# Kernel tuning notes

Measured on AMD Instinct MI355X. Metric: run time of the kernel, lower is better.

The kernel has to match this reference:

```python
import jax, jax.numpy as jnp
import numpy as np

N_NODES = 100000
N_EDGES = 3200000
D_IN, D_HID, D_OUT = 128, 128, 128


def setup_inputs() -> dict:
    key = jax.random.key(0)
    ks = jax.random.split(key, 8)
    x = jax.random.normal(ks[0], (N_NODES, D_IN), dtype=jnp.float32)
    edge_index = jax.random.randint(ks[1], (2, N_EDGES), 0, N_NODES, dtype=jnp.int64)
    def lin(k, din, dout):
        # glorot-ish init for GCNConv weight
        s = 1.0 / np.sqrt(din)
        return jax.random.uniform(k, (din, dout), jnp.float32, -s, s)
    W0 = lin(ks[2], D_IN, D_HID)
    b0 = jnp.zeros((D_HID,), jnp.float32)
    W1 = lin(ks[3], D_HID, D_HID)
    b1 = jnp.zeros((D_HID,), jnp.float32)
    W2 = lin(ks[4], D_HID, D_OUT)
    b2 = jnp.zeros((D_OUT,), jnp.float32)
    return {"x": x, "edge_index": edge_index, "W0": W0, "b0": b0,
            "W1": W1, "b1": b1, "W2": W2, "b2": b2}


def _gcn_norm(edge_index, n_nodes):
    # PyG gcn_norm with self-loops: deg over target index, sym normalization
    loop = jnp.arange(n_nodes, dtype=edge_index.dtype)
    src = jnp.concatenate([edge_index[0], loop])
    dst = jnp.concatenate([edge_index[1], loop])
    deg = jax.ops.segment_sum(jnp.ones_like(dst, dtype=jnp.float32), dst,
                              num_segments=n_nodes)
    dinv = jnp.where(deg > 0, jax.lax.rsqrt(deg), 0.0)
    norm = dinv[src] * dinv[dst]  # [E + N]
    return src, dst, norm


def _gcn_conv(h, src, dst, norm, W, b, n_nodes):
    h = h @ W                                   # [N, dout] transform first
    msg = h[src] * norm[:, None]                # gather + scale
    out = jax.ops.segment_sum(msg, dst, num_segments=n_nodes)  # scatter-add
    return out + b


def reference(x, edge_index, W0, b0, W1, b1, W2, b2):
    n = x.shape[0]
    src, dst, norm = _gcn_norm(edge_index, n)
    # layer 0
    h = jax.nn.relu(_gcn_conv(x, src, dst, norm, W0, b0, n))
    # residual middle layer (dropout is identity in eval mode)
    h = jax.nn.relu(_gcn_conv(h, src, dst, norm, W1, b1, n) + h)
    # output layer
    return _gcn_conv(h, src, dst, norm, W2, b2, n)
```

## Files before the change

### kernel.cpp

```cpp
#include <hip/hip_runtime.h>
#include <hip/hip_fp16.h>

#define D 128
typedef unsigned long long ull;
typedef _Float16 half8 __attribute__((ext_vector_type(8)));
typedef _Float16 half4v __attribute__((ext_vector_type(4)));
typedef float f32x4 __attribute__((ext_vector_type(4)));

#define KPOS(k4) (((k4) & ~31) + ((((k4) & 15) >> 2) << 3) + ((((k4) >> 4) & 1) << 2))

__global__ void k_zero_int(int* p, int n) {
  int i = blockIdx.x * blockDim.x + threadIdx.x;
  if (i < n) p[i] = 0;
}

__global__ void k_deg_count8(const int* __restrict__ ei, int* __restrict__ deg8,
                             int E, int N) {
  int e = blockIdx.x * blockDim.x + threadIdx.x;
  if (e >= E) return;
  int d = __builtin_nontemporal_load(&ei[E + e]);
  atomicAdd(&deg8[(blockIdx.x & 7) * N + d], 1);
}

__global__ void k_deg_reduce(const int* __restrict__ deg8, int* __restrict__ deg, int N) {
  int i = blockIdx.x * blockDim.x + threadIdx.x;
  if (i >= N) return;
  int s = 0;
#pragma unroll
  for (int c = 0; c < 8; c++) s += deg8[c * N + i];
  deg[i] = s;
}

__global__ void k_scan_part(const int* __restrict__ deg, int* __restrict__ part, int n) {
  __shared__ int sd[256];
  int base = blockIdx.x * 2048 + threadIdx.x * 8;
  int s = 0;
#pragma unroll
  for (int k = 0; k < 8; k++) {
    int idx = base + k;
    if (idx < n) s += deg[idx];
  }
  sd[threadIdx.x] = s;
  __syncthreads();
  for (int off = 128; off > 0; off >>= 1) {
    if (threadIdx.x < off) sd[threadIdx.x] += sd[threadIdx.x + off];
    __syncthreads();
  }
  if (threadIdx.x == 0) part[blockIdx.x] = sd[0];
}

__global__ void k_scan_offsets(int* __restrict__ part, int nparts,
                               int* __restrict__ rowptr, int n) {
  __shared__ int sd[256];
  int v = (threadIdx.x < nparts) ? part[threadIdx.x] : 0;
  sd[threadIdx.x] = v;
  __syncthreads();
  for (int off = 1; off < 256; off <<= 1) {
    int t = (threadIdx.x >= off) ? sd[threadIdx.x - off] : 0;
    __syncthreads();
    sd[threadIdx.x] += t;
    __syncthreads();
  }
  if (threadIdx.x < nparts) part[threadIdx.x] = sd[threadIdx.x] - v;
  if (threadIdx.x == 0) rowptr[n] = sd[255];
}

__global__ void k_scan_final(const int* __restrict__ deg, const int* __restrict__ part,
                             int* __restrict__ rowptr, int n) {
  __shared__ int sd[256];
  int base = blockIdx.x * 2048 + threadIdx.x * 8;
  int loc[8];
  int s = 0;
#pragma unroll
  for (int k = 0; k < 8; k++) {
    int idx = base + k;
    loc[k] = (idx < n) ? deg[idx] : 0;
    s += loc[k];
  }
  sd[threadIdx.x] = s;
  __syncthreads();
  for (int off = 1; off < 256; off <<= 1) {
    int t = (threadIdx.x >= off) ? sd[threadIdx.x - off] : 0;
    __syncthreads();
    sd[threadIdx.x] += t;
    __syncthreads();
  }
  int run = part[blockIdx.x] + sd[threadIdx.x] - s;
#pragma unroll
  for (int k = 0; k < 8; k++) {
    int idx = base + k;
    if (idx < n) {
      rowptr[idx] = run;
      run += loc[k];
    }
  }
}

__global__ void k_dinv_cursor(const int* __restrict__ rowptr, float* __restrict__ dinv,
                              int* __restrict__ cursor, int n) {
  int i = blockIdx.x * blockDim.x + threadIdx.x;
  if (i < n) {
    int r0 = rowptr[i], r1 = rowptr[i + 1];
    dinv[i] = rsqrtf((float)(r1 - r0) + 1.0f);
    cursor[i] = r0;
  }
}

__global__ void k_csr_fill_x(const int* __restrict__ ei, int* __restrict__ cursor,
                             int* __restrict__ csr, int E, int bsz) {
  const int bucket = blockIdx.x & 7;
  const int slice = blockIdx.x >> 3;
  const int nsl = gridDim.x >> 3;
  const int lo = bucket * bsz;
  const int chunk = (E + nsl - 1) / nsl;
  const int start = slice * chunk;
  int endE = start + chunk;
  if (endE > E) endE = E;
  for (int e = start + threadIdx.x; e < endE; e += 256) {
    int d = __builtin_nontemporal_load(&ei[E + e]);
    if ((unsigned)(d - lo) < (unsigned)bsz) {
      int s = __builtin_nontemporal_load(&ei[e]);
      int pos = atomicAdd(&cursor[d], 1);
      csr[pos] = s;
    }
  }
}

template <int HALF_IN>
__launch_bounds__(256, 2)
__global__ void k_gemm_mfma(const void* __restrict__ Av, const float* __restrict__ W,
                            const float* __restrict__ dinv, __half* __restrict__ Th, int n) {
  __shared__ _Float16 Al[128 * 136];
  __shared__ _Float16 Bl[128 * 136];
  const int tid = threadIdx.x;
  const int row0 = blockIdx.x * 128;

  if (HALF_IN) {
    const _Float16* A = (const _Float16*)Av;
    for (int i = tid; i < 2048; i += 256) {
      int r = i >> 4;
      int k8 = (i & 15) << 3;
      half8 v = {0, 0, 0, 0, 0, 0, 0, 0};
      if (row0 + r < n) v = *(const half8*)&A[(size_t)(row0 + r) * D + k8];
      *(half4v*)&Al[r * 136 + KPOS(k8)]     = (half4v){v[0], v[1], v[2], v[3]};
      *(half4v*)&Al[r * 136 + KPOS(k8 + 4)] = (half4v){v[4], v[5], v[6], v[7]};
    }
  } else {
    const float* A = (const float*)Av;
    for (int i = tid; i < 4096; i += 256) {
      int r = i >> 5;
      int k4 = (i & 31) << 2;
      float4 v = make_float4(0.f, 0.f, 0.f, 0.f);
      if (row0 + r < n) v = ((const float4*)A)[(size_t)(row0 + r) * 32 + (i & 31)];
      *(half4v*)&Al[r * 136 + KPOS(k4)] =
          (half4v){(_Float16)v.x, (_Float16)v.y, (_Float16)v.z, (_Float16)v.w};
    }
  }
  for (int i = tid; i < 4096; i += 256) {
    int c = i & 127;
    int k4 = (i >> 7) << 2;
    float w0 = W[(k4 + 0) * D + c];
    float w1 = W[(k4 + 1) * D + c];
    float w2 = W[(k4 + 2) * D + c];
    float w3 = W[(k4 + 3) * D + c];
    *(half4v*)&Bl[c * 136 + KPOS(k4)] =
        (half4v){(_Float16)w0, (_Float16)w1, (_Float16)w2, (_Float16)w3};
  }
  __syncthreads();

  const int w = tid >> 6;
  const int lane = tid & 63;
  const int g = lane >> 4;
  const int q = lane & 15;

  f32x4 acc[2][8];
#pragma unroll
  for (int mt = 0; mt < 2; mt++)
#pragma unroll
    for (int nt = 0; nt < 8; nt++) acc[mt][nt] = (f32x4){0.f, 0.f, 0.f, 0.f};

#pragma unroll
  for (int kt = 0; kt < 4; kt++) {
    half8 a[2], b[8];
#pragma unroll
    for (int mt = 0; mt < 2; mt++)
      a[mt] = *(const half8*)&Al[(w * 32 + mt * 16 + q) * 136 + kt * 32 + g * 8];
#pragma unroll
    for (int nt = 0; nt < 8; nt++)
      b[nt] = *(const half8*)&Bl[(nt * 16 + q) * 136 + kt * 32 + g * 8];
#pragma unroll
    for (int mt = 0; mt < 2; mt++)
#pragma unroll
      for (int nt = 0; nt < 8; nt++)
        acc[mt][nt] = __builtin_amdgcn_mfma_f32_16x16x32_f16(a[mt], b[nt], acc[mt][nt], 0, 0, 0);
  }

#pragma unroll
  for (int mt = 0; mt < 2; mt++) {
    int baseRow = row0 + w * 32 + mt * 16 + g * 4;
    float dv[4];
#pragma unroll
    for (int r = 0; r < 4; r++) dv[r] = (baseRow + r < n) ? dinv[baseRow + r] : 0.f;
#pragma unroll
    for (int nt = 0; nt < 8; nt++) {
      int col = nt * 16 + q;
#pragma unroll
      for (int r = 0; r < 4; r++) {
        int gr = baseRow + r;
        if (gr < n) Th[(size_t)gr * D + col] = (__half)(acc[mt][nt][r] * dv[r]);
      }
    }
  }
}

template <int MODE>
__launch_bounds__(256)
__global__ void k_aggregate(const int* __restrict__ rowptr, const int* __restrict__ csr,
                            const float* __restrict__ dinv, const __half* __restrict__ th,
                            const float* __restrict__ b, const __half* __restrict__ resh,
                            __half* __restrict__ outh, float* __restrict__ outf, int n) {
  int node = blockIdx.x * 16 + (threadIdx.x >> 4);
  if (node >= n) return;
  const int l16 = threadIdx.x & 15;

  int beg = rowptr[node];
  int end = rowptr[node + 1];
  float dd = dinv[node];

  const float4* t4 = (const float4*)th;

  float a0, a1, a2, a3, a4, a5, a6, a7;
  {
    float4 raw = t4[(size_t)node * 16 + l16];
    const __half2* hp = (const __half2*)&raw;
    float2 f0 = __half22float2(hp[0]);
    float2 f1 = __half22float2(hp[1]);
    float2 f2 = __half22float2(hp[2]);
    float2 f3 = __half22float2(hp[3]);
    a0 = f0.x; a1 = f0.y; a2 = f1.x; a3 = f1.y;
    a4 = f2.x; a5 = f2.y; a6 = f3.x; a7 = f3.y;
  }

#define ACC_ROW(raw)                                  \
  {                                                   \
    const __half2* hp = (const __half2*)&(raw);       \
    float2 f0 = __half22float2(hp[0]);                \
    float2 f1 = __half22float2(hp[1]);                \
    float2 f2 = __half22float2(hp[2]);                \
    float2 f3 = __half22float2(hp[3]);                \
    a0 += f0.x; a1 += f0.y; a2 += f1.x; a3 += f1.y;   \
    a4 += f2.x; a5 += f2.y; a6 += f3.x; a7 += f3.y;   \
  }

  int j = beg;
  for (; j + 8 <= end; j += 8) {
    float4 r0, r1, r2, r3, r4, r5, r6, r7;
    {
      int s0 = __builtin_nontemporal_load(&csr[j + 0]);
      int s1 = __builtin_nontemporal_load(&csr[j + 1]);
      int s2 = __builtin_nontemporal_load(&csr[j + 2]);
      int s3 = __builtin_nontemporal_load(&csr[j + 3]);
      int s4 = __builtin_nontemporal_load(&csr[j + 4]);
      int s5 = __builtin_nontemporal_load(&csr[j + 5]);
      int s6 = __builtin_nontemporal_load(&csr[j + 6]);
      int s7 = __builtin_nontemporal_load(&csr[j + 7]);
      r0 = t4[(size_t)(unsigned)s0 * 16 + l16];
      r1 = t4[(size_t)(unsigned)s1 * 16 + l16];
      r2 = t4[(size_t)(unsigned)s2 * 16 + l16];
      r3 = t4[(size_t)(unsigned)s3 * 16 + l16];
      r4 = t4[(size_t)(unsigned)s4 * 16 + l16];
      r5 = t4[(size_t)(unsigned)s5 * 16 + l16];
      r6 = t4[(size_t)(unsigned)s6 * 16 + l16];
      r7 = t4[(size_t)(unsigned)s7 * 16 + l16];
    }
    ACC_ROW(r0) ACC_ROW(r1) ACC_ROW(r2) ACC_ROW(r3)
    ACC_ROW(r4) ACC_ROW(r5) ACC_ROW(r6) ACC_ROW(r7)
  }
  for (; j + 4 <= end; j += 4) {
    int s0 = __builtin_nontemporal_load(&csr[j + 0]);
    int s1 = __builtin_nontemporal_load(&csr[j + 1]);
    int s2 = __builtin_nontemporal_load(&csr[j + 2]);
    int s3 = __builtin_nontemporal_load(&csr[j + 3]);
    float4 r0 = t4[(size_t)(unsigned)s0 * 16 + l16];
    float4 r1 = t4[(size_t)(unsigned)s1 * 16 + l16];
    float4 r2 = t4[(size_t)(unsigned)s2 * 16 + l16];
    float4 r3 = t4[(size_t)(unsigned)s3 * 16 + l16];
    ACC_ROW(r0) ACC_ROW(r1) ACC_ROW(r2) ACC_ROW(r3)
  }
  for (; j < end; ++j) {
    int s = __builtin_nontemporal_load(&csr[j]);
    float4 r = t4[(size_t)(unsigned)s * 16 + l16];
    ACC_ROW(r)
  }
#undef ACC_ROW

  const float4* b4 = (const float4*)b;
  float4 bb0 = b4[l16 * 2];
  float4 bb1 = b4[l16 * 2 + 1];
  float o0 = fmaf(a0, dd, bb0.x), o1 = fmaf(a1, dd, bb0.y);
  float o2 = fmaf(a2, dd, bb0.z), o3 = fmaf(a3, dd, bb0.w);
  float o4 = fmaf(a4, dd, bb1.x), o5 = fmaf(a5, dd, bb1.y);
  float o6 = fmaf(a6, dd, bb1.z), o7 = fmaf(a7, dd, bb1.w);

  if (MODE == 1) {
    float4 raw = ((const float4*)resh)[(size_t)node * 16 + l16];
    const __half2* hp = (const __half2*)&raw;
    float2 f0 = __half22float2(hp[0]);
    float2 f1 = __half22float2(hp[1]);
    float2 f2 = __half22float2(hp[2]);
    float2 f3 = __half22float2(hp[3]);
    o0 += f0.x; o1 += f0.y; o2 += f1.x; o3 += f1.y;
    o4 += f2.x; o5 += f2.y; o6 += f3.x; o7 += f3.y;
  }
  if (MODE == 0 || MODE == 1) {
    o0 = fmaxf(o0, 0.f); o1 = fmaxf(o1, 0.f); o2 = fmaxf(o2, 0.f); o3 = fmaxf(o3, 0.f);
    o4 = fmaxf(o4, 0.f); o5 = fmaxf(o5, 0.f); o6 = fmaxf(o6, 0.f); o7 = fmaxf(o7, 0.f);
    union { __half2 h[4]; float4 f; } pk;
    pk.h[0] = __floats2half2_rn(o0, o1);
    pk.h[1] = __floats2half2_rn(o2, o3);
    pk.h[2] = __floats2half2_rn(o4, o5);
    pk.h[3] = __floats2half2_rn(o6, o7);
    ((float4*)outh)[(size_t)node * 16 + l16] = pk.f;
  } else {
    ((float4*)outf)[(size_t)node * 32 + l16 * 2] = make_float4(o0, o1, o2, o3);
    ((float4*)outf)[(size_t)node * 32 + l16 * 2 + 1] = make_float4(o4, o5, o6, o7);
  }
}

extern "C" void kernel_launch(void* const* d_in, const int* in_sizes, int n_in,
                              void* d_out, int out_size, void* d_ws, size_t ws_size,
                              hipStream_t stream) {
  const float* x  = (const float*)d_in[0];
  const int*   ei = (const int*)d_in[1];
  const float* W0 = (const float*)d_in[2];
  const float* b0 = (const float*)d_in[3];
  const float* W1 = (const float*)d_in[4];
  const float* b1 = (const float*)d_in[5];
  const float* W2 = (const float*)d_in[6];
  const float* b2 = (const float*)d_in[7];
  float* out = (float*)d_out;

  const int N = in_sizes[0] / D;
  const int E = in_sizes[1] / 2;

  char* wsb = (char*)d_ws;
  auto alloc = [&](size_t bytes) {
    char* p = wsb;
    wsb += ((bytes + 255) & ~(size_t)255);
    return p;
  };
  int*    rowptr = (int*)alloc((N + 1) * 4);
  int*    cursor = (int*)alloc(N * 4);
  int*    part   = (int*)alloc(256 * 4);
  float*  dinv   = (float*)alloc(N * 4);
  int*    deg8   = (int*)alloc((size_t)8 * N * 4);
  int*    csr    = (int*)alloc((size_t)E * 4);
  __half* th     = (__half*)alloc((size_t)N * D * 2);
  __half* g1h    = (__half*)alloc((size_t)N * D * 2);
  __half* g2h    = (__half*)alloc((size_t)N * D * 2);

  dim3 b256(256);
  int gN   = (N + 255) / 256;
  int gN8  = (8 * N + 255) / 256;
  int gE   = (E + 255) / 256;
  int gGem = (N + 127) / 128;
  int gAgg = (N + 15) / 16;
  int nparts = (N + 2047) / 2048;

  int* deg = cursor;
  k_zero_int<<<gN8, b256, 0, stream>>>(deg8, 8 * N);
  k_deg_count8<<<gE, b256, 0, stream>>>(ei, deg8, E, N);
  k_deg_reduce<<<gN, b256, 0, stream>>>(deg8, deg, N);
  k_scan_part<<<nparts, b256, 0, stream>>>(deg, part, N);
  k_scan_offsets<<<1, b256, 0, stream>>>(part, nparts, rowptr, N);
  k_scan_final<<<nparts, b256, 0, stream>>>(deg, part, rowptr, N);
  k_dinv_cursor<<<gN, b256, 0, stream>>>(rowptr, dinv, cursor, N);
  int bsz = (N + 7) / 8;
  k_csr_fill_x<<<8 * 256, b256, 0, stream>>>(ei, cursor, csr, E, bsz);

  k_gemm_mfma<0><<<gGem, b256, 0, stream>>>(x, W0, dinv, th, N);
  k_aggregate<0><<<gAgg, b256, 0, stream>>>(rowptr, csr, dinv, th, b0, nullptr, g1h, nullptr, N);

  k_gemm_mfma<1><<<gGem, b256, 0, stream>>>(g1h, W1, dinv, th, N);
  k_aggregate<1><<<gAgg, b256, 0, stream>>>(rowptr, csr, dinv, th, b1, g1h, g2h, nullptr, N);

  k_gemm_mfma<1><<<gGem, b256, 0, stream>>>(g2h, W2, dinv, th, N);
  k_aggregate<2><<<gAgg, b256, 0, stream>>>(rowptr, csr, dinv, th, b2, nullptr, nullptr, out, N);
}
```

Before: 746.3 us.

## Build CSR in one pass using per-chunk degree counts as sub-cursors

```diff
diff --git a/kernel.cpp b/kernel.cpp
--- a/kernel.cpp
+++ b/kernel.cpp
@@ -16,10 +16,18 @@
 
 __global__ void k_deg_count8(const int* __restrict__ ei, int* __restrict__ deg8,
                              int E, int N) {
-  int e = blockIdx.x * blockDim.x + threadIdx.x;
-  if (e >= E) return;
-  int d = __builtin_nontemporal_load(&ei[E + e]);
-  atomicAdd(&deg8[(blockIdx.x & 7) * N + d], 1);
+  const int c = blockIdx.x & 7;
+  const int m = blockIdx.x >> 3;
+  const int nb = gridDim.x >> 3;
+  const int cE = (E + 7) >> 3;
+  const int base = c * cE;
+  int lim = E - base;
+  if (lim > cE) lim = cE;
+  int* dg = deg8 + (size_t)c * N;
+  for (int i = m * 256 + threadIdx.x; i < lim; i += nb * 256) {
+    int d = __builtin_nontemporal_load(&ei[E + base + i]);
+    atomicAdd(&dg[d], 1);
+  }
 }
 
 __global__ void k_deg_reduce(const int* __restrict__ deg8, int* __restrict__ deg, int N) {
@@ -27,7 +35,7 @@
   if (i >= N) return;
   int s = 0;
 #pragma unroll
-  for (int c = 0; c < 8; c++) s += deg8[c * N + i];
+  for (int c = 0; c < 8; c++) s += deg8[(size_t)c * N + i];
   deg[i] = s;
 }
 
@@ -96,33 +104,38 @@
   }
 }
 
-__global__ void k_dinv_cursor(const int* __restrict__ rowptr, float* __restrict__ dinv,
-                              int* __restrict__ cursor, int n) {
+__global__ void k_dinv(const int* __restrict__ rowptr, float* __restrict__ dinv, int n) {
   int i = blockIdx.x * blockDim.x + threadIdx.x;
-  if (i < n) {
-    int r0 = rowptr[i], r1 = rowptr[i + 1];
-    dinv[i] = rsqrtf((float)(r1 - r0) + 1.0f);
-    cursor[i] = r0;
-  }
-}
-
-__global__ void k_csr_fill_x(const int* __restrict__ ei, int* __restrict__ cursor,
-                             int* __restrict__ csr, int E, int bsz) {
-  const int bucket = blockIdx.x & 7;
-  const int slice = blockIdx.x >> 3;
-  const int nsl = gridDim.x >> 3;
-  const int lo = bucket * bsz;
-  const int chunk = (E + nsl - 1) / nsl;
-  const int start = slice * chunk;
-  int endE = start + chunk;
-  if (endE > E) endE = E;
-  for (int e = start + threadIdx.x; e < endE; e += 256) {
-    int d = __builtin_nontemporal_load(&ei[E + e]);
-    if ((unsigned)(d - lo) < (unsigned)bsz) {
-      int s = __builtin_nontemporal_load(&ei[e]);
-      int pos = atomicAdd(&cursor[d], 1);
-      csr[pos] = s;
-    }
+  if (i < n) dinv[i] = rsqrtf((float)(rowptr[i + 1] - rowptr[i]) + 1.0f);
+}
+
+__global__ void k_cursor8_init(const int* __restrict__ rowptr, const int* __restrict__ deg8,
+                               int* __restrict__ cursor8, int N) {
+  int v = blockIdx.x * blockDim.x + threadIdx.x;
+  if (v >= N) return;
+  int run = rowptr[v];
+#pragma unroll
+  for (int c = 0; c < 8; c++) {
+    cursor8[(size_t)c * N + v] = run;
+    run += deg8[(size_t)c * N + v];
+  }
+}
+
+__global__ void k_csr_fill_1p(const int* __restrict__ ei, int* __restrict__ cursor8,
+                              int* __restrict__ csr, int E, int N) {
+  const int c = blockIdx.x & 7;
+  const int m = blockIdx.x >> 3;
+  const int nb = gridDim.x >> 3;
+  const int cE = (E + 7) >> 3;
+  const int base = c * cE;
+  int lim = E - base;
+  if (lim > cE) lim = cE;
+  int* cur = cursor8 + (size_t)c * N;
+  for (int i = m * 256 + threadIdx.x; i < lim; i += nb * 256) {
+    int d = __builtin_nontemporal_load(&ei[E + base + i]);
+    int s = __builtin_nontemporal_load(&ei[base + i]);
+    int pos = atomicAdd(&cur[d], 1);
+    csr[pos] = s;
   }
 }
 
@@ -349,34 +362,33 @@
     wsb += ((bytes + 255) & ~(size_t)255);
     return p;
   };
-  int*    rowptr = (int*)alloc((N + 1) * 4);
-  int*    cursor = (int*)alloc(N * 4);
-  int*    part   = (int*)alloc(256 * 4);
-  float*  dinv   = (float*)alloc(N * 4);
-  int*    deg8   = (int*)alloc((size_t)8 * N * 4);
-  int*    csr    = (int*)alloc((size_t)E * 4);
-  __half* th     = (__half*)alloc((size_t)N * D * 2);
-  __half* g1h    = (__half*)alloc((size_t)N * D * 2);
-  __half* g2h    = (__half*)alloc((size_t)N * D * 2);
+  int*    rowptr  = (int*)alloc((N + 1) * 4);
+  int*    deg     = (int*)alloc(N * 4);
+  int*    part    = (int*)alloc(256 * 4);
+  float*  dinv    = (float*)alloc(N * 4);
+  int*    deg8    = (int*)alloc((size_t)8 * N * 4);
+  int*    cursor8 = (int*)alloc((size_t)8 * N * 4);
+  int*    csr     = (int*)alloc((size_t)E * 4);
+  __half* th      = (__half*)alloc((size_t)N * D * 2);
+  __half* g1h     = (__half*)alloc((size_t)N * D * 2);
+  __half* g2h     = (__half*)alloc((size_t)N * D * 2);
 
   dim3 b256(256);
   int gN   = (N + 255) / 256;
   int gN8  = (8 * N + 255) / 256;
-  int gE   = (E + 255) / 256;
   int gGem = (N + 127) / 128;
   int gAgg = (N + 15) / 16;
   int nparts = (N + 2047) / 2048;
 
-  int* deg = cursor;
   k_zero_int<<<gN8, b256, 0, stream>>>(deg8, 8 * N);
-  k_deg_count8<<<gE, b256, 0, stream>>>(ei, deg8, E, N);
+  k_deg_count8<<<8 * 256, b256, 0, stream>>>(ei, deg8, E, N);
   k_deg_reduce<<<gN, b256, 0, stream>>>(deg8, deg, N);
   k_scan_part<<<nparts, b256, 0, stream>>>(deg, part, N);
   k_scan_offsets<<<1, b256, 0, stream>>>(part, nparts, rowptr, N);
   k_scan_final<<<nparts, b256, 0, stream>>>(deg, part, rowptr, N);
-  k_dinv_cursor<<<gN, b256, 0, stream>>>(rowptr, dinv, cursor, N);
-  int bsz = (N + 7) / 8;
-  k_csr_fill_x<<<8 * 256, b256, 0, stream>>>(ei, cursor, csr, E, bsz);
+  k_dinv<<<gN, b256, 0, stream>>>(rowptr, dinv, N);
+  k_cursor8_init<<<gN, b256, 0, stream>>>(rowptr, deg8, cursor8, N);
+  k_csr_fill_1p<<<8 * 256, b256, 0, stream>>>(ei, cursor8, csr, E, N);
 
   k_gemm_mfma<0><<<gGem, b256, 0, stream>>>(x, W0, dinv, th, N);
   k_aggregate<0><<<gAgg, b256, 0, stream>>>(rowptr, csr, dinv, th, b0, nullptr, g1h, nullptr, N);
```

Result: slower. 819.1 us (+9.8%).
